# Performance work log

Hardware: AMD Instinct MI355X
Metric: run time of the kernel (lower is better)

The kernel has to match this reference:

```python
import jax, jax.numpy as jnp
import numpy as np

B, T = 32, 512
LATENT, COND, HIDDEN, OUT, E = 64, 448, 1024, 512, 8
INPUT = LATENT + COND            # 512
INTER = LATENT + COND + HIDDEN   # 1536
GATE_H = 64


def setup_inputs() -> dict:
    key = jax.random.key(0)
    ks = jax.random.split(key, 20)
    d = {
        "z": jax.random.normal(ks[0], (B, T, LATENT), dtype=jnp.float32),
        "c": jax.random.normal(ks[1], (B, T, COND), dtype=jnp.float32),
    }
    # expert weights: kaiming-uniform-ish init, biases filled with 0.01 (as in torch code)
    layer_dims = [(INPUT, HIDDEN), (INTER, HIDDEN), (INTER, HIDDEN), (INTER, HIDDEN), (INTER, OUT)]
    for i, (fin, fout) in enumerate(layer_dims):
        bound = float(np.sqrt(6.0 / fin))
        d[f"w{i}"] = jax.random.uniform(ks[2 + i], (E, fin, fout), dtype=jnp.float32, minval=-bound, maxval=bound)
        d[f"b{i}"] = jnp.full((E, fout), 0.01, dtype=jnp.float32)
    # gate MLP: input_size -> 64 -> 64 -> E (stored as [in, out])
    gate_dims = [(INPUT, GATE_H), (GATE_H, GATE_H), (GATE_H, E)]
    for i, (fin, fout) in enumerate(gate_dims):
        bound = float(np.sqrt(1.0 / fin))
        d[f"gw{i}"] = jax.random.uniform(ks[10 + 2 * i], (fin, fout), dtype=jnp.float32, minval=-bound, maxval=bound)
        d[f"gb{i}"] = jax.random.uniform(ks[11 + 2 * i], (fout,), dtype=jnp.float32, minval=-bound, maxval=bound)
    return d


def reference(z, c, w0, b0, w1, b1, w2, b2, w3, b3, w4, b4, gw0, gb0, gw1, gb1, gw2, gb2):
    # gate -> per-token softmax mixing coefficients  [B, T, E]
    x = jnp.concatenate([z, c], axis=-1)
    h = jax.nn.leaky_relu(x @ gw0 + gb0)
    h = jax.nn.leaky_relu(h @ gw1 + gb1)
    coef = jax.nn.softmax(h @ gw2 + gb2, axis=-1)
    # Original computes mixed_weight for every t but baddbmm uses only mixed_weight[:, 0];
    # so the effective per-sequence weight uses coefficients at t=0 only (same math, no huge intermediate).
    coef0 = coef[:, 0]  # [B, E]
    layer_out = c
    layers = [(w0, b0, True), (w1, b1, True), (w2, b2, True), (w3, b3, True), (w4, b4, False)]
    for i, (w, b, act) in enumerate(layers):
        if i == 0:
            inp = jnp.concatenate([z, layer_out], axis=-1)      # [B, T, INPUT]
        else:
            inp = jnp.concatenate([z, c, layer_out], axis=-1)   # [B, T, INTER]
        wm = jnp.einsum('be,eio->bio', coef0, w)                # per-sequence mixed weight
        bm = jnp.einsum('bte,eo->bto', coef, b)                 # per-token mixed bias
        out = bm + jnp.einsum('bti,bio->bto', inp, wm)
        layer_out = jax.nn.leaky_relu(out) if act else out
    return layer_out
```

## Files before the change

kernel.cpp:

```cpp
#include <hip/hip_runtime.h>
#include <math.h>

#define B_     32
#define T_     512
#define LATENT 64
#define COND   448
#define HIDDEN 1024
#define OUTD   512
#define E_     8
#define INPUT_ 512
#define INTER_ 1536
#define GATEH  64
#define NTOK   (B_ * T_)
#define KTAIL  32

typedef __attribute__((ext_vector_type(8))) short short8;
typedef __attribute__((ext_vector_type(4))) float f32x4;

static __device__ __forceinline__ unsigned short f2bf(float x) {
    unsigned u = __float_as_uint(x);
    u += 0x7fffu + ((u >> 16) & 1u);
    return (unsigned short)(u >> 16);
}

__global__ __launch_bounds__(256) void wprep_kernel(
    const float* __restrict__ gw0, const float* __restrict__ gw1,
    unsigned short* __restrict__ gw0T, unsigned short* __restrict__ gw1T)
{
    int idx = blockIdx.x * 256 + threadIdx.x;
    if (idx < GATEH * INPUT_) {
        int n = idx >> 9, k = idx & 511;
        gw0T[n * INPUT_ + k] = f2bf(gw0[k * GATEH + n]);
    } else {
        int i2 = idx - GATEH * INPUT_;
        if (i2 < GATEH * GATEH) {
            int n = i2 >> 6, k = i2 & 63;
            gw1T[n * GATEH + k] = f2bf(gw1[k * GATEH + n]);
        }
    }
}

__global__ __launch_bounds__(256) void gate_kernel(
    const float* __restrict__ z, const float* __restrict__ c,
    const float* __restrict__ gb0,
    const float* __restrict__ gb1,
    const float* __restrict__ gw2, const float* __restrict__ gb2,
    const unsigned short* __restrict__ gw0T,
    const unsigned short* __restrict__ gw1T,
    float* __restrict__ coef, unsigned short* __restrict__ coefpad,
    unsigned short* __restrict__ xzb)
{
    __shared__ unsigned short Hb[GATEH][72];
    __shared__ float H2[GATEH][65];
    __shared__ float sLg[GATEH][E_];

    const int tid = threadIdx.x;
    const int lane = tid & 63;
    const int wv = tid >> 6;
    const int tok0 = blockIdx.x * 64;

#pragma unroll
    for (int i = 0; i < 4; ++i) {
        int idx = i * 256 + tid;
        int tr = idx >> 4, c4 = (idx & 15) * 4;
        float4 v = *(const float4*)(z + ((size_t)(tok0 + tr) * LATENT) + c4);
        ushort4 o = {f2bf(v.x), f2bf(v.y), f2bf(v.z), f2bf(v.w)};
        *(ushort4*)(xzb + (size_t)(tok0 + tr) * INPUT_ + c4) = o;
    }
#pragma unroll
    for (int i = 0; i < 28; ++i) {
        int idx = i * 256 + tid;
        int tr = idx / 112, c4 = (idx % 112) * 4;
        float4 v = *(const float4*)(c + ((size_t)(tok0 + tr) * COND) + c4);
        ushort4 o = {f2bf(v.x), f2bf(v.y), f2bf(v.z), f2bf(v.w)};
        *(ushort4*)(xzb + (size_t)(tok0 + tr) * INPUT_ + LATENT + c4) = o;
    }
    __threadfence_block();
    __syncthreads();

    const int fr = lane & 15, fq = lane >> 4;
    const int wm0 = (wv & 1) * 32, wn0 = (wv >> 1) * 32;

    f32x4 acc[2][2];
#pragma unroll
    for (int im = 0; im < 2; ++im)
#pragma unroll
        for (int in = 0; in < 2; ++in) acc[im][in] = (f32x4){0.f,0.f,0.f,0.f};

    for (int k0 = 0; k0 < INPUT_; k0 += 32) {
        short8 af[2], bf[2];
#pragma unroll
        for (int im = 0; im < 2; ++im)
            af[im] = *(const short8*)(xzb + (size_t)(tok0 + wm0 + im*16 + fr) * INPUT_
                                          + k0 + fq * 8);
#pragma unroll
        for (int in = 0; in < 2; ++in)
            bf[in] = *(const short8*)(gw0T + (size_t)(wn0 + in*16 + fr) * INPUT_
                                           + k0 + fq * 8);
#pragma unroll
        for (int im = 0; im < 2; ++im)
#pragma unroll
            for (int in = 0; in < 2; ++in)
                acc[im][in] = __builtin_amdgcn_mfma_f32_16x16x32_bf16(
                    af[im], bf[in], acc[im][in], 0, 0, 0);
    }
#pragma unroll
    for (int im = 0; im < 2; ++im)
#pragma unroll
        for (int in = 0; in < 2; ++in)
#pragma unroll
            for (int reg = 0; reg < 4; ++reg) {
                int m = wm0 + im*16 + fq*4 + reg;
                int n = wn0 + in*16 + fr;
                float h = acc[im][in][reg] + gb0[n];
                h = h > 0.f ? h : 0.01f * h;
                Hb[m][n] = f2bf(h);
            }
    __syncthreads();

    f32x4 a2[2][2];
#pragma unroll
    for (int im = 0; im < 2; ++im)
#pragma unroll
        for (int in = 0; in < 2; ++in) a2[im][in] = (f32x4){0.f,0.f,0.f,0.f};
#pragma unroll
    for (int k0 = 0; k0 < GATEH; k0 += 32) {
        short8 af[2], bf[2];
#pragma unroll
        for (int im = 0; im < 2; ++im)
            af[im] = *(const short8*)(&Hb[wm0 + im*16 + fr][k0 + fq*8]);
#pragma unroll
        for (int in = 0; in < 2; ++in)
            bf[in] = *(const short8*)(gw1T + (size_t)(wn0 + in*16 + fr) * GATEH
                                           + k0 + fq * 8);
#pragma unroll
        for (int im = 0; im < 2; ++im)
#pragma unroll
            for (int in = 0; in < 2; ++in)
                a2[im][in] = __builtin_amdgcn_mfma_f32_16x16x32_bf16(
                    af[im], bf[in], a2[im][in], 0, 0, 0);
    }
#pragma unroll
    for (int im = 0; im < 2; ++im)
#pragma unroll
        for (int in = 0; in < 2; ++in)
#pragma unroll
            for (int reg = 0; reg < 4; ++reg) {
                int m = wm0 + im*16 + fq*4 + reg;
                int n = wn0 + in*16 + fr;
                float h = a2[im][in][reg] + gb1[n];
                H2[m][n] = h > 0.f ? h : 0.01f * h;
            }
    __syncthreads();

    {
        int tok = tid >> 2, e0 = (tid & 3) * 2;
        float l0 = gb2[e0], l1 = gb2[e0 + 1];
#pragma unroll
        for (int i = 0; i < GATEH; ++i) {
            float h = H2[tok][i];
            l0 = fmaf(h, gw2[i * E_ + e0], l0);
            l1 = fmaf(h, gw2[i * E_ + e0 + 1], l1);
        }
        sLg[tok][e0] = l0; sLg[tok][e0 + 1] = l1;
    }
    __syncthreads();

    if (tid < 64) {
        int token = tok0 + tid;
        float lg[E_], m = -1e30f, s = 0.f;
#pragma unroll
        for (int e = 0; e < E_; ++e) { lg[e] = sLg[tid][e]; m = fmaxf(m, lg[e]); }
#pragma unroll
        for (int e = 0; e < E_; ++e) { lg[e] = expf(lg[e] - m); s += lg[e]; }
        float inv = 1.f / s;
        unsigned short pad[KTAIL];
#pragma unroll
        for (int e = 0; e < E_; ++e) {
            float cv = lg[e] * inv;
            coef[(size_t)token * E_ + e] = cv;
            pad[e] = f2bf(cv);
        }
#pragma unroll
        for (int j = E_; j < KTAIL; ++j) pad[j] = 0;
#pragma unroll
        for (int q = 0; q < 4; ++q)
            *(ushort4*)(coefpad + (size_t)token * KTAIL + q * 4) =
                *(const ushort4*)&pad[q * 4];
    }
}

#define MI 32
#define MO 64
#define MP 65

__global__ __launch_bounds__(256) void mixT_kernel(
    const float* __restrict__ w,
    const float* __restrict__ bias,
    const float* __restrict__ coef,
    unsigned short* __restrict__ wmT,
    int fin, int fout, int gb, int batch0)
{
    __shared__ float sW[E_][MI][MP];
    __shared__ float sC[B_][E_];
    const int t = threadIdx.x;
    const int fin_tot = fin + KTAIL;
    const int nbi = fin / MI;
    const int i0 = (blockIdx.x % nbi) * MI;
    const int o0 = (blockIdx.x / nbi) * MO;

    if (t < gb * E_)
        sC[t >> 3][t & 7] = coef[(size_t)(batch0 + (t >> 3)) * T_ * E_ + (t & 7)];

#pragma unroll
    for (int r = 0; r < 64; ++r) {
        int idx = r * 256 + t;
        int o = idx & 63;
        int i = (idx >> 6) & 31;
        int e = idx >> 11;
        sW[e][i][o] = w[(size_t)e * fin * fout + (size_t)(i0 + i) * fout + o0 + o];
    }
    __syncthreads();

    const int o  = t >> 2;
    const int i8 = (t & 3) * 8;
    for (int b = 0; b < gb; ++b) {
        float v[8];
#pragma unroll
        for (int j = 0; j < 8; ++j) v[j] = 0.f;
#pragma unroll
        for (int e = 0; e < E_; ++e) {
            float cc = sC[b][e];
#pragma unroll
            for (int j = 0; j < 8; ++j)
                v[j] = fmaf(cc, sW[e][i8 + j][o], v[j]);
        }
        unsigned short u[8];
#pragma unroll
        for (int j = 0; j < 8; ++j) u[j] = f2bf(v[j]);
        *(int4*)(wmT + ((size_t)b * fout + o0 + o) * fin_tot + i0 + i8) = *(const int4*)u;
    }

    if (i0 == 0) {
        const int jj = t & 3;
        unsigned short u[8];
#pragma unroll
        for (int q = 0; q < 8; ++q)
            u[q] = (jj == 0) ? f2bf(bias[(size_t)q * fout + o0 + o]) : 0;
        for (int b = 0; b < gb; ++b)
            *(int4*)(wmT + ((size_t)b * fout + o0 + o) * fin_tot + fin + jj * 8) =
                *(const int4*)u;
    }
}

__global__ __launch_bounds__(256, 3) void gemm_kernel(
    const unsigned short* __restrict__ xz,
    const unsigned short* __restrict__ prev,
    const unsigned short* __restrict__ wmT,
    const unsigned short* __restrict__ coefpad,
    float* __restrict__ outf,
    unsigned short* __restrict__ outb,
    int fin_tot, int fout, int act, int batch0)
{
    __shared__ __align__(16) unsigned short As[128 * 32];
    __shared__ __align__(16) unsigned short Bs[128 * 32];

    const int tid = threadIdx.x;
    const int lane = tid & 63;
    const int wv = tid >> 6;
    const int row0 = blockIdx.y * 128;
    const int col0 = blockIdx.x * 128;
    const size_t tokbase = (size_t)(batch0 + blockIdx.z) * T_;
    const unsigned short* wmb = wmT + (size_t)blockIdx.z * fin_tot * fout;

    f32x4 acc[4][4];
#pragma unroll
    for (int im = 0; im < 4; ++im)
#pragma unroll
        for (int in = 0; in < 4; ++in)
            acc[im][in] = (f32x4){0.f, 0.f, 0.f, 0.f};

    const int lrow = lane >> 2;
    const int lk8  = (((lane & 3) ^ ((lane >> 3) & 3)) * 8);
    const int wm0 = (wv & 1) * 64, wn0 = (wv >> 1) * 64;
    const int fr = lane & 15, fq = lane >> 4;
    const int koff = (fq ^ ((fr >> 1) & 3)) * 8;
    const int ktail0 = fin_tot - KTAIL;

    for (int k0 = 0; k0 < fin_tot; k0 += 32) {
        const unsigned short* abase; int astr, acol;
        if (k0 < INPUT_)       { abase = xz;      astr = INPUT_; acol = k0; }
        else if (k0 < ktail0)  { abase = prev;    astr = HIDDEN; acol = k0 - INPUT_; }
        else                   { abase = coefpad; astr = KTAIL;  acol = 0; }

        __syncthreads();
#pragma unroll
        for (int q = 0; q < 4; ++q) {
            int ch = wv * 4 + q;
            const unsigned short* src;
            unsigned short* dst;
            if (ch < 8) {
                int m = ch * 16 + lrow;
                src = abase + (tokbase + row0 + m) * astr + acol + lk8;
                dst = As + ch * 512;
            } else {
                int n = (ch - 8) * 16 + lrow;
                src = wmb + (size_t)(col0 + n) * fin_tot + k0 + lk8;
                dst = Bs + (ch - 8) * 512;
            }
            __builtin_amdgcn_global_load_lds(
                (const __attribute__((address_space(1))) unsigned int*)(const void*)src,
                (__attribute__((address_space(3))) unsigned int*)(void*)dst,
                16, 0, 0);
        }
        __syncthreads();

        short8 af[4], bfv[4];
#pragma unroll
        for (int im = 0; im < 4; ++im)
            af[im] = *(const short8*)(As + (wm0 / 16 + im) * 512 + fr * 32 + koff);
#pragma unroll
        for (int in = 0; in < 4; ++in)
            bfv[in] = *(const short8*)(Bs + (wn0 / 16 + in) * 512 + fr * 32 + koff);
#pragma unroll
        for (int im = 0; im < 4; ++im)
#pragma unroll
            for (int in = 0; in < 4; ++in)
                acc[im][in] = __builtin_amdgcn_mfma_f32_16x16x32_bf16(
                    af[im], bfv[in], acc[im][in], 0, 0, 0);
    }

#pragma unroll
    for (int im = 0; im < 4; ++im) {
#pragma unroll
        for (int in = 0; in < 4; ++in) {
#pragma unroll
            for (int reg = 0; reg < 4; ++reg) {
                int r = wm0 + im * 16 + fq * 4 + reg;
                int col = wn0 + in * 16 + fr;
                float v = acc[im][in][reg];
                if (act) v = v > 0.f ? v : 0.01f * v;
                size_t off = (tokbase + row0 + r) * fout + col0 + col;
                if (outb) outb[off] = f2bf(v);
                else      outf[off] = v;
            }
        }
    }
}

extern "C" void kernel_launch(void* const* d_in, const int* in_sizes, int n_in,
                              void* d_out, int out_size, void* d_ws, size_t ws_size,
                              hipStream_t stream)
{
    const float* z = (const float*)d_in[0];
    const float* c = (const float*)d_in[1];
    const float* w[5]  = {(const float*)d_in[2], (const float*)d_in[4],
                          (const float*)d_in[6], (const float*)d_in[8],
                          (const float*)d_in[10]};
    const float* bs[5] = {(const float*)d_in[3], (const float*)d_in[5],
                          (const float*)d_in[7], (const float*)d_in[9],
                          (const float*)d_in[11]};
    const float* gw0 = (const float*)d_in[12]; const float* gb0 = (const float*)d_in[13];
    const float* gw1 = (const float*)d_in[14]; const float* gb1 = (const float*)d_in[15];
    const float* gw2 = (const float*)d_in[16]; const float* gb2 = (const float*)d_in[17];

    const size_t g0t_b  = (size_t)GATEH * INPUT_ * 2;
    const size_t g1t_b  = (size_t)GATEH * GATEH * 2;
    const size_t xz_b   = (size_t)NTOK * INPUT_ * 2;
    const size_t coef_b = (size_t)NTOK * E_ * 4;
    const size_t cpad_b = (size_t)NTOK * KTAIL * 2;
    const size_t act_b  = (size_t)NTOK * HIDDEN * 2;
    const size_t wmun   = (size_t)(INTER_ + KTAIL) * HIDDEN * 2;

    char* p = (char*)d_ws;
    unsigned short* gw0T  = (unsigned short*)p;  p += g0t_b;
    unsigned short* gw1T  = (unsigned short*)p;  p += g1t_b;
    unsigned short* xzb   = (unsigned short*)p;  p += xz_b;
    float*          coef  = (float*)p;           p += coef_b;
    unsigned short* cpad  = (unsigned short*)p;  p += cpad_b;
    unsigned short* actB  = (unsigned short*)p;  p += act_b;

    size_t base = g0t_b + g1t_b + xz_b + coef_b + cpad_b + act_b;
    size_t avail = (ws_size > base) ? ws_size - base : 0;

    int gb;
    unsigned short* actA;
    unsigned short* wmT;
    if (avail >= act_b + 32 * wmun) {
        gb = 32; actA = (unsigned short*)p; p += act_b; wmT = (unsigned short*)p;
    } else {
        actA = (unsigned short*)d_out;
        wmT  = (unsigned short*)p;
        gb = 1;
        for (int g = 16; g >= 2; g >>= 1)
            if (avail >= (size_t)g * wmun) { gb = g; break; }
    }

    wprep_kernel<<<(GATEH * (INPUT_ + GATEH) + 255) / 256, 256, 0, stream>>>(
        gw0, gw1, gw0T, gw1T);
    gate_kernel<<<NTOK / 64, 256, 0, stream>>>(
        z, c, gb0, gb1, gw2, gb2, gw0T, gw1T, coef, cpad, xzb);

    struct L { int fin, fout, act; const unsigned short* in; unsigned short* outb; };
    L Ls[5] = {
        {INPUT_, HIDDEN, 1, actB , actA},
        {INTER_, HIDDEN, 1, actA, actB},
        {INTER_, HIDDEN, 1, actB, actA},
        {INTER_, HIDDEN, 1, actA, actB},
        {INTER_, OUTD,   0, actB, 0},
    };

    for (int Li = 0; Li < 5; ++Li) {
        int fin = Ls[Li].fin, fout = Ls[Li].fout;
        int nblk = (fin / MI) * (fout / MO);
        for (int g = 0; g < B_; g += gb) {
            mixT_kernel<<<nblk, 256, 0, stream>>>(
                w[Li], bs[Li], coef, wmT, fin, fout, gb, g);
            gemm_kernel<<<dim3(fout / 128, T_ / 128, gb), 256, 0, stream>>>(
                xzb, Ls[Li].in, wmT, cpad,
                (float*)d_out, Ls[Li].outb, fin + KTAIL, fout, Ls[Li].act, g);
        }
    }
}
```

Baseline: 717.3 us.

## Enlarge GEMM tiles to 256x256 with 4-stage async LDS pipeline and XCD swizzle

The bf16 GEMM moves from 128x128 tiles with 256 threads to 256x256 tiles with 512 threads. It adds a 4-deep ring of LDS buffers filled by async global_load_lds, using vmcnt-based waits so loads overlap the MFMA work, and raises wave priority around the MFMA block. Workgroup ids are remapped round-robin across 8 chiplets to improve L2 locality. In exchange it uses much more LDS and more accumulator registers per thread, and the larger tiles mean fewer blocks per launch.

```diff
diff --git a/kernel.cpp b/kernel.cpp
--- a/kernel.cpp
+++ b/kernel.cpp
@@ -253,7 +253,7 @@
     }
 }
 
-__global__ __launch_bounds__(256, 3) void gemm_kernel(
+__global__ __launch_bounds__(512, 2) void gemm_kernel(
     const unsigned short* __restrict__ xz,
     const unsigned short* __restrict__ prev,
     const unsigned short* __restrict__ wmT,
@@ -262,82 +262,119 @@
     unsigned short* __restrict__ outb,
     int fin_tot, int fout, int act, int batch0)
 {
-    __shared__ __align__(16) unsigned short As[128 * 32];
-    __shared__ __align__(16) unsigned short Bs[128 * 32];
+    __shared__ __align__(16) unsigned short As[4][8192];
+    __shared__ __align__(16) unsigned short Bs[4][8192];
 
     const int tid = threadIdx.x;
     const int lane = tid & 63;
-    const int wv = tid >> 6;
-    const int row0 = blockIdx.y * 128;
-    const int col0 = blockIdx.x * 128;
-    const size_t tokbase = (size_t)(batch0 + blockIdx.z) * T_;
-    const unsigned short* wmb = wmT + (size_t)blockIdx.z * fin_tot * fout;
-
-    f32x4 acc[4][4];
-#pragma unroll
-    for (int im = 0; im < 4; ++im)
-#pragma unroll
-        for (int in = 0; in < 4; ++in)
-            acc[im][in] = (f32x4){0.f, 0.f, 0.f, 0.f};
+    const int w8 = tid >> 6;
+    const int wm = w8 & 1;
+    const int wn = w8 >> 1;
+
+    const int nx = gridDim.x;
+    int bx = blockIdx.x, by = blockIdx.y, bz = blockIdx.z;
+    {
+        int nwg = nx * 2 * gridDim.z;
+        if ((nwg & 7) == 0) {
+            int f = blockIdx.x + nx * (blockIdx.y + 2 * blockIdx.z);
+            int q = nwg >> 3;
+            int wk = (f & 7) * q + (f >> 3);
+            int bpb = nx * 2;
+            bz = wk / bpb;
+            int r = wk - bz * bpb;
+            by = r / nx;
+            bx = r - by * nx;
+        }
+    }
+
+    const int row0 = by * 256;
+    const int col0 = bx * 256;
+    const size_t tokbase = (size_t)(batch0 + bz) * T_;
+    const unsigned short* wmb = wmT + (size_t)bz * fin_tot * fout;
 
     const int lrow = lane >> 2;
     const int lk8  = (((lane & 3) ^ ((lane >> 3) & 3)) * 8);
-    const int wm0 = (wv & 1) * 64, wn0 = (wv >> 1) * 64;
     const int fr = lane & 15, fq = lane >> 4;
     const int koff = (fq ^ ((fr >> 1) & 3)) * 8;
     const int ktail0 = fin_tot - KTAIL;
-
-    for (int k0 = 0; k0 < fin_tot; k0 += 32) {
+    const int nt = fin_tot >> 5;
+
+    f32x4 acc[8][4];
+#pragma unroll
+    for (int im = 0; im < 8; ++im)
+#pragma unroll
+        for (int in = 0; in < 4; ++in)
+            acc[im][in] = (f32x4){0.f, 0.f, 0.f, 0.f};
+
+    auto stage = [&](int t) {
+        int k0 = t << 5;
         const unsigned short* abase; int astr, acol;
-        if (k0 < INPUT_)       { abase = xz;      astr = INPUT_; acol = k0; }
-        else if (k0 < ktail0)  { abase = prev;    astr = HIDDEN; acol = k0 - INPUT_; }
-        else                   { abase = coefpad; astr = KTAIL;  acol = 0; }
-
-        __syncthreads();
-#pragma unroll
-        for (int q = 0; q < 4; ++q) {
-            int ch = wv * 4 + q;
-            const unsigned short* src;
-            unsigned short* dst;
-            if (ch < 8) {
-                int m = ch * 16 + lrow;
-                src = abase + (tokbase + row0 + m) * astr + acol + lk8;
-                dst = As + ch * 512;
-            } else {
-                int n = (ch - 8) * 16 + lrow;
-                src = wmb + (size_t)(col0 + n) * fin_tot + k0 + lk8;
-                dst = Bs + (ch - 8) * 512;
-            }
+        if (k0 < INPUT_)      { abase = xz;      astr = INPUT_; acol = k0; }
+        else if (k0 < ktail0) { abase = prev;    astr = HIDDEN; acol = k0 - INPUT_; }
+        else                  { abase = coefpad; astr = KTAIL;  acol = 0; }
+        unsigned short* Ab = As[t & 3];
+        unsigned short* Bb = Bs[t & 3];
+#pragma unroll
+        for (int j = 0; j < 2; ++j) {
+            int ch = w8 + 8 * j;
+            const unsigned short* srcA = abase
+                + (tokbase + row0 + ch * 16 + lrow) * (size_t)astr + acol + lk8;
             __builtin_amdgcn_global_load_lds(
-                (const __attribute__((address_space(1))) unsigned int*)(const void*)src,
-                (__attribute__((address_space(3))) unsigned int*)(void*)dst,
+                (const __attribute__((address_space(1))) unsigned int*)(const void*)srcA,
+                (__attribute__((address_space(3))) unsigned int*)(void*)(Ab + ch * 512),
                 16, 0, 0);
-        }
-        __syncthreads();
-
-        short8 af[4], bfv[4];
-#pragma unroll
-        for (int im = 0; im < 4; ++im)
-            af[im] = *(const short8*)(As + (wm0 / 16 + im) * 512 + fr * 32 + koff);
+            const unsigned short* srcB = wmb
+                + (size_t)(col0 + ch * 16 + lrow) * fin_tot + k0 + lk8;
+            __builtin_amdgcn_global_load_lds(
+                (const __attribute__((address_space(1))) unsigned int*)(const void*)srcB,
+                (__attribute__((address_space(3))) unsigned int*)(void*)(Bb + ch * 512),
+                16, 0, 0);
+        }
+    };
+
+    stage(0);
+    if (nt > 1) stage(1);
+    if (nt > 2) stage(2);
+
+    for (int t = 0; t < nt; ++t) {
+        int rem = nt - 1 - t;
+        if (rem >= 2)
+            asm volatile("s_waitcnt vmcnt(8)\n\ts_barrier" ::: "memory");
+        else if (rem == 1)
+            asm volatile("s_waitcnt vmcnt(4)\n\ts_barrier" ::: "memory");
+        else
+            asm volatile("s_waitcnt vmcnt(0)\n\ts_barrier" ::: "memory");
+
+        if (t + 3 < nt) stage(t + 3);
+
+        const unsigned short* Ab = As[t & 3] + wm * 4096;
+        const unsigned short* Bb = Bs[t & 3] + wn * 2048;
+        short8 af[8], bfv[4];
+#pragma unroll
+        for (int im = 0; im < 8; ++im)
+            af[im] = *(const short8*)(Ab + im * 512 + fr * 32 + koff);
 #pragma unroll
         for (int in = 0; in < 4; ++in)
-            bfv[in] = *(const short8*)(Bs + (wn0 / 16 + in) * 512 + fr * 32 + koff);
-#pragma unroll
-        for (int im = 0; im < 4; ++im)
+            bfv[in] = *(const short8*)(Bb + in * 512 + fr * 32 + koff);
+
+        __builtin_amdgcn_s_setprio(1);
+#pragma unroll
+        for (int im = 0; im < 8; ++im)
 #pragma unroll
             for (int in = 0; in < 4; ++in)
                 acc[im][in] = __builtin_amdgcn_mfma_f32_16x16x32_bf16(
                     af[im], bfv[in], acc[im][in], 0, 0, 0);
-    }
-
-#pragma unroll
-    for (int im = 0; im < 4; ++im) {
+        __builtin_amdgcn_s_setprio(0);
+    }
+
+#pragma unroll
+    for (int im = 0; im < 8; ++im) {
 #pragma unroll
         for (int in = 0; in < 4; ++in) {
 #pragma unroll
             for (int reg = 0; reg < 4; ++reg) {
-                int r = wm0 + im * 16 + fq * 4 + reg;
-                int col = wn0 + in * 16 + fr;
+                int r = wm * 128 + im * 16 + fq * 4 + reg;
+                int col = wn * 64 + in * 16 + fr;
                 float v = acc[im][in][reg];
                 if (act) v = v > 0.f ? v : 0.01f * v;
                 size_t off = (tokbase + row0 + r) * fout + col0 + col;
@@ -416,7 +453,7 @@
         for (int g = 0; g < B_; g += gb) {
             mixT_kernel<<<nblk, 256, 0, stream>>>(
                 w[Li], bs[Li], coef, wmT, fin, fout, gb, g);
-            gemm_kernel<<<dim3(fout / 128, T_ / 128, gb), 256, 0, stream>>>(
+            gemm_kernel<<<dim3(fout / 256, T_ / 256, gb), 512, 0, stream>>>(
                 xzb, Ls[Li].in, wmT, cpad,
                 (float*)d_out, Ls[Li].outb, fin + KTAIL, fout, Ls[Li].act, g);
         }
```

New measurement: 698.4 us. -2.6%, faster.
